# Kernel optimization log

Measured on AMD Instinct MI355X. Metric: run time of the kernel, lower is better.

The kernel has to match this reference:

```python
import jax, jax.numpy as jnp
import numpy as np


def setup_inputs() -> dict:
    key = jax.random.key(0)
    ks = jax.random.split(key, 5)
    B, C, H, W = 32, 32, 64, 64   # latent feature map (latent_space_channel_dim=32)
    D, K = 32, 512                # quant_dim, codebook_size
    return {
        "z": jax.random.normal(ks[0], (B, C, H, W), jnp.float32),
        "quant_w": jax.random.normal(ks[1], (D, C), jnp.float32) * 0.1,   # 1x1 conv kernel
        "quant_b": jnp.zeros((D,), jnp.float32),
        "codebook": jax.random.normal(ks[2], (K, D), jnp.float32),
        "post_quant_w": jax.random.normal(ks[3], (C, D), jnp.float32) * 0.1,
        "post_quant_b": jnp.zeros((C,), jnp.float32),
    }


def reference(z, quant_w, quant_b, codebook, post_quant_w, post_quant_b):
    B, C, H, W = z.shape
    D = quant_w.shape[0]
    # quant_conv: 1x1 conv == channel GEMM
    x = jnp.einsum('bchw,dc->bdhw', z, quant_w) + quant_b[None, :, None, None]
    # rearrange 'b c h w -> b c (h w)' then flatten tokens to [B*HW, D]
    xf = x.transpose(0, 2, 3, 1).reshape(-1, D)
    # squared euclidean distances to codebook (cdist**2), argmin, gather
    d2 = (jnp.sum(xf * xf, axis=-1, keepdims=True)
          - 2.0 * (xf @ codebook.T)
          + jnp.sum(codebook * codebook, axis=-1)[None, :])  # [B*HW, K]
    idx = jnp.argmin(d2, axis=-1)                              # [B*HW]
    q = codebook[idx]                                          # gather [B*HW, D]
    # commitment loss (encoder pull) + codebook loss (learnable codebook, no EMA)
    commit = jnp.mean((jax.lax.stop_gradient(q) - xf) ** 2)
    cb_loss = jnp.mean((q - jax.lax.stop_gradient(xf)) ** 2)
    loss = commit + cb_loss
    # straight-through estimator
    q_st = xf + jax.lax.stop_gradient(q - xf)
    qmap = q_st.reshape(B, H, W, D).transpose(0, 3, 1, 2)      # 'b c (h w) -> b c h w'
    # post_quant_conv: 1x1 conv back to latent channels
    out = jnp.einsum('bdhw,cd->bchw', qmap, post_quant_w) + post_quant_b[None, :, None, None]
    return out, idx.reshape(B, H * W), loss
```

## Files before the change

kernel.cpp:

```cpp
#include <hip/hip_runtime.h>

#define C_    32
#define D_    32
#define K_    512
#define HW_   4096
#define NTOK  131072
#define IDX_OFF   4194304
#define LOSS_OFF  4325376
#define TAU      2e-3f
#define CONS_EPS 1e-3f

#define WS_CBN   0
#define WS_CBH   4096
#define WS_CBL   36864
#define WS_XH    69632
#define WS_XL    8458240
#define WS_XFT   16846848
#define WS_IDXF  33624064
#define WS_BESTW 34148352
#define WS_NEEDED 34672640

typedef __attribute__((ext_vector_type(8))) __bf16 bf16x8;
typedef __attribute__((ext_vector_type(8))) short  short8;
typedef __attribute__((ext_vector_type(4))) float  f32x4;

__device__ inline unsigned short f2bf(float x) {
    unsigned u = __builtin_bit_cast(unsigned, x);
    return (unsigned short)((u + 0x7FFFu + ((u >> 16) & 1u)) >> 16);
}
__device__ inline float bf2f(unsigned short h) {
    unsigned u = ((unsigned)h) << 16; return __builtin_bit_cast(float, u);
}
__device__ inline bf16x8 ldfrag(const unsigned short* p) {
    return __builtin_bit_cast(bf16x8, *(const short8*)p);
}

__global__ __launch_bounds__(256)
void prep(const float* __restrict__ z,  const float* __restrict__ qw,
          const float* __restrict__ qb, const float* __restrict__ cb,
          float* __restrict__ cbn, unsigned short* __restrict__ cbh,
          unsigned short* __restrict__ cbl, unsigned short* __restrict__ xh,
          unsigned short* __restrict__ xl, float* __restrict__ xfT)
{
    const int tid = threadIdx.x;
    if (blockIdx.x == 0) {
        for (int k = tid; k < K_; k += 256) {
            const float* row = cb + k * D_;
            float s = 0.f; unsigned short hrow[32], lrow[32];
            #pragma unroll
            for (int d = 0; d < D_; ++d) {
                float v = row[d]; s = fmaf(v, v, s);
                unsigned short h = f2bf(v); hrow[d] = h; lrow[d] = f2bf(v - bf2f(h));
            }
            cbn[k] = s;
            #pragma unroll
            for (int j = 0; j < 4; ++j) {
                *(short8*)(cbh + k * 32 + 8 * j) = *(const short8*)(hrow + 8 * j);
                *(short8*)(cbl + k * 32 + 8 * j) = *(const short8*)(lrow + 8 * j);
            }
        }
    }
    const int token = blockIdx.x * 256 + tid;
    const int b = token >> 12, hw = token & (HW_ - 1);
    const float* zbase = z + (size_t)b * (C_ * HW_) + hw;
    float zv[C_];
    #pragma unroll
    for (int c = 0; c < C_; ++c) zv[c] = zbase[(size_t)c * HW_];
    unsigned short hrow[32], lrow[32];
    #pragma unroll
    for (int d = 0; d < D_; ++d) {
        float a = qb[d]; const float* qr = qw + d * C_;
        #pragma unroll
        for (int c = 0; c < C_; ++c) a = fmaf(zv[c], qr[c], a);
        xfT[(size_t)d * NTOK + token] = a;
        unsigned short h = f2bf(a); hrow[d] = h; lrow[d] = f2bf(a - bf2f(h));
    }
    #pragma unroll
    for (int j = 0; j < 4; ++j) {
        *(short8*)(xh + (size_t)token * 32 + 8 * j) = *(const short8*)(hrow + 8 * j);
        *(short8*)(xl + (size_t)token * 32 + 8 * j) = *(const short8*)(lrow + 8 * j);
    }
}

__global__ __launch_bounds__(256)
void scan_mfma(const unsigned short* __restrict__ xh, const unsigned short* __restrict__ xl,
               const unsigned short* __restrict__ cbh, const unsigned short* __restrict__ cbl,
               const float* __restrict__ cbn, unsigned* __restrict__ idxf,
               float* __restrict__ bestW)
{
    const int tid = threadIdx.x;
    const int wv = tid >> 6, l = tid & 63;
    const int tile = (blockIdx.x * 4 + wv) * 32;
    const int lr = l & 15, lg = l >> 4;

    const unsigned short* pa  = xh + (size_t)(tile + lr) * 32 + lg * 8;
    const unsigned short* pal = xl + (size_t)(tile + lr) * 32 + lg * 8;
    bf16x8 ah0 = ldfrag(pa),  ah1 = ldfrag(pa + 16 * 32);
    bf16x8 al0 = ldfrag(pal), al1 = ldfrag(pal + 16 * 32);

    float b1[8], b2[8]; int i1[8];
    #pragma unroll
    for (int s = 0; s < 8; ++s) { b1[s] = 3.4e38f; b2[s] = 3.4e38f; i1[s] = 0; }

    #pragma unroll 2
    for (int nt = 0; nt < 32; ++nt) {
        const size_t boff = (size_t)(nt * 16 + lr) * 32 + lg * 8;
        bf16x8 bh = ldfrag(cbh + boff);
        bf16x8 bl = ldfrag(cbl + boff);
        const float cn = cbn[nt * 16 + lr];
        f32x4 acc0 = {0.f, 0.f, 0.f, 0.f}, acc1 = {0.f, 0.f, 0.f, 0.f};
        acc0 = __builtin_amdgcn_mfma_f32_16x16x32_bf16(ah0, bh, acc0, 0, 0, 0);
        acc0 = __builtin_amdgcn_mfma_f32_16x16x32_bf16(ah0, bl, acc0, 0, 0, 0);
        acc0 = __builtin_amdgcn_mfma_f32_16x16x32_bf16(al0, bh, acc0, 0, 0, 0);
        acc1 = __builtin_amdgcn_mfma_f32_16x16x32_bf16(ah1, bh, acc1, 0, 0, 0);
        acc1 = __builtin_amdgcn_mfma_f32_16x16x32_bf16(ah1, bl, acc1, 0, 0, 0);
        acc1 = __builtin_amdgcn_mfma_f32_16x16x32_bf16(al1, bh, acc1, 0, 0, 0);
        const int n = nt * 16 + lr;
        #pragma unroll
        for (int r = 0; r < 4; ++r) {
            {
                const float d2 = fmaf(-2.f, acc0[r], cn);
                const bool lt1 = d2 < b1[r], lt2 = d2 < b2[r];
                b2[r] = lt1 ? b1[r] : (lt2 ? d2 : b2[r]);
                b1[r] = lt1 ? d2 : b1[r];
                i1[r] = lt1 ? n  : i1[r];
            }
            {
                const float d2 = fmaf(-2.f, acc1[r], cn);
                const bool lt1 = d2 < b1[4+r], lt2 = d2 < b2[4+r];
                b2[4+r] = lt1 ? b1[4+r] : (lt2 ? d2 : b2[4+r]);
                b1[4+r] = lt1 ? d2 : b1[4+r];
                i1[4+r] = lt1 ? n  : i1[4+r];
            }
        }
    }
    #pragma unroll
    for (int mk = 1; mk < 16; mk <<= 1) {
        #pragma unroll
        for (int s = 0; s < 8; ++s) {
            const float ob1 = __shfl_xor(b1[s], mk);
            const int   oi1 = __shfl_xor(i1[s], mk);
            const float ob2 = __shfl_xor(b2[s], mk);
            const bool take = (ob1 < b1[s]) || (ob1 == b1[s] && oi1 < i1[s]);
            const float loser = take ? b1[s] : ob1;
            b1[s] = take ? ob1 : b1[s];
            i1[s] = take ? oi1 : i1[s];
            b2[s] = fminf(fminf(b2[s], ob2), loser);
        }
    }
    #pragma unroll
    for (int s = 0; s < 8; ++s) {
        if (lr == s) {
            const int token = tile + (s >> 2) * 16 + lg * 4 + (s & 3);
            const bool fl = (b2[s] - b1[s]) < TAU;
            idxf[token]  = (unsigned)i1[s] | (fl ? 0x80000000u : 0u);
            bestW[token] = b1[s];
        }
    }
}

__global__ __launch_bounds__(256)
void combine(const float* __restrict__ cb, const float* __restrict__ pw,
             const float* __restrict__ pb, const float* __restrict__ cbn,
             const float* __restrict__ xfT, const unsigned* __restrict__ idxf,
             const float* __restrict__ bestW, float* __restrict__ out)
{
    __shared__ float lsum[4];
    const int tid = threadIdx.x;
    const int token = blockIdx.x * 256 + tid;
    const int b = token >> 12, hw = token & (HW_ - 1);
    const int lane = tid & 63;

    const unsigned pf = idxf[token];
    int idx = (int)(pf & 511u);
    int flag = (int)(pf >> 31);

    float xf[D_];
    #pragma unroll
    for (int d = 0; d < D_; ++d) xf[d] = xfT[(size_t)d * NTOK + token];

    {
        const float* row = cb + (size_t)idx * D_;
        float p0 = 0.f, p1 = 0.f, p2 = 0.f, p3 = 0.f;
        #pragma unroll
        for (int d = 0; d < D_; d += 4) {
            p0 = fmaf(xf[d],   row[d],   p0); p1 = fmaf(xf[d+1], row[d+1], p1);
            p2 = fmaf(xf[d+2], row[d+2], p2); p3 = fmaf(xf[d+3], row[d+3], p3);
        }
        const float dd = fmaf(-2.f, (p0 + p1) + (p2 + p3), cbn[idx]);
        flag |= (fabsf(dd - bestW[token]) > CONS_EPS) ? 1 : 0;
    }

    unsigned long long m = __ballot(flag != 0);
    while (m) {
        const int j = __ffsll(m) - 1; m &= m - 1;
        const int tokj = blockIdx.x * 256 + (tid & ~63) + j;
        float xfj[D_];
        #pragma unroll
        for (int d = 0; d < D_; ++d) xfj[d] = xfT[(size_t)d * NTOK + tokj];
        float bb = 3.4e38f; int bi = 0;
        #pragma unroll
        for (int p = 0; p < 8; ++p) {
            const int c = lane + 64 * p;
            const float* row = cb + (size_t)c * D_;
            float p0 = 0.f, p1 = 0.f, p2 = 0.f, p3 = 0.f;
            #pragma unroll
            for (int d = 0; d < D_; d += 4) {
                p0 = fmaf(xfj[d],   row[d],   p0); p1 = fmaf(xfj[d+1], row[d+1], p1);
                p2 = fmaf(xfj[d+2], row[d+2], p2); p3 = fmaf(xfj[d+3], row[d+3], p3);
            }
            const float dd = fmaf(-2.f, (p0 + p1) + (p2 + p3), cbn[c]);
            if (dd < bb) { bb = dd; bi = c; }
        }
        #pragma unroll
        for (int s = 1; s < 64; s <<= 1) {
            const float ob = __shfl_xor(bb, s); const int oi = __shfl_xor(bi, s);
            if (ob < bb || (ob == bb && oi < bi)) { bb = ob; bi = oi; }
        }
        if (lane == j) idx = bi;
    }

    out[IDX_OFF + token] = (float)idx;

    const float* qrow = cb + (size_t)idx * D_;
    float qv[D_], l = 0.f;
    #pragma unroll
    for (int d = 0; d < D_; ++d) { qv[d] = qrow[d]; const float df = qv[d] - xf[d]; l = fmaf(df, df, l); }

    float* obase = out + (size_t)b * (C_ * HW_) + hw;
    #pragma unroll
    for (int c = 0; c < C_; ++c) {
        float a = pb[c]; const float* pr = pw + c * D_;
        #pragma unroll
        for (int d = 0; d < D_; ++d) a = fmaf(qv[d], pr[d], a);
        obase[(size_t)c * HW_] = a;
    }

    #pragma unroll
    for (int off = 32; off; off >>= 1) l += __shfl_down(l, off);
    const int wid = tid >> 6;
    if (lane == 0) lsum[wid] = l;
    __syncthreads();
    if (tid == 0)
        atomicAdd(out + LOSS_OFF, ((lsum[0] + lsum[1]) + (lsum[2] + lsum[3])) * (2.0f / (float)(NTOK * D_)));
}

__global__ __launch_bounds__(256)
void vq_mono(const float* __restrict__ z,  const float* __restrict__ qw,
             const float* __restrict__ qb, const float* __restrict__ cb,
             const float* __restrict__ pw, const float* __restrict__ pb,
             float* __restrict__ out)
{
    __shared__ float cbn_s[K_];
    __shared__ float lsum[4];
    const int tid = threadIdx.x;
    for (int k = tid; k < K_; k += 256) {
        const float* row = cb + k * D_;
        float s = 0.f;
        #pragma unroll
        for (int d = 0; d < D_; ++d) s = fmaf(row[d], row[d], s);
        cbn_s[k] = s;
    }
    __syncthreads();
    const int token = blockIdx.x * 256 + tid;
    const int b = token >> 12, hw = token & (HW_ - 1);
    const float* zbase = z + (size_t)b * C_ * HW_ + hw;
    float zv[C_];
    #pragma unroll
    for (int c = 0; c < C_; ++c) zv[c] = zbase[(size_t)c * HW_];
    float xf[D_];
    #pragma unroll
    for (int d = 0; d < D_; ++d) {
        float a = qb[d];
        #pragma unroll
        for (int c = 0; c < C_; ++c) a = fmaf(zv[c], qw[d * C_ + c], a);
        xf[d] = a;
    }
    float best = 3.4e38f; int bi = 0;
    #pragma unroll 2
    for (int k = 0; k < K_; ++k) {
        const float* row = cb + k * D_;
        float p0 = 0.f, p1 = 0.f, p2 = 0.f, p3 = 0.f;
        #pragma unroll
        for (int d = 0; d < D_; d += 4) {
            p0 = fmaf(xf[d+0], row[d+0], p0); p1 = fmaf(xf[d+1], row[d+1], p1);
            p2 = fmaf(xf[d+2], row[d+2], p2); p3 = fmaf(xf[d+3], row[d+3], p3);
        }
        const float s = fmaf(-2.f, (p0+p1)+(p2+p3), cbn_s[k]);
        if (s < best) { best = s; bi = k; }
    }
    out[IDX_OFF + token] = (float)bi;
    const float* qrow = cb + (size_t)bi * D_;
    float qv[D_];
    #pragma unroll
    for (int d = 0; d < D_; ++d) qv[d] = qrow[d];
    float l = 0.f;
    #pragma unroll
    for (int d = 0; d < D_; ++d) { const float df = qv[d] - xf[d]; l = fmaf(df, df, l); }
    float* obase = out + (size_t)b * C_ * HW_ + hw;
    #pragma unroll
    for (int c = 0; c < C_; ++c) {
        float a = pb[c];
        #pragma unroll
        for (int d = 0; d < D_; ++d) a = fmaf(qv[d], pw[c * D_ + d], a);
        obase[(size_t)c * HW_] = a;
    }
    #pragma unroll
    for (int off = 32; off; off >>= 1) l += __shfl_down(l, off);
    const int wid = tid >> 6, lane = tid & 63;
    if (lane == 0) lsum[wid] = l;
    __syncthreads();
    if (tid == 0) {
        const float t = (lsum[0] + lsum[1]) + (lsum[2] + lsum[3]);
        atomicAdd(out + LOSS_OFF, t * (2.0f / (float)(NTOK * D_)));
    }
}

extern "C" void kernel_launch(void* const* d_in, const int* in_sizes, int n_in,
                              void* d_out, int out_size, void* d_ws, size_t ws_size,
                              hipStream_t stream) {
    (void)in_sizes; (void)n_in; (void)out_size;
    const float* z  = (const float*)d_in[0];
    const float* qw = (const float*)d_in[1];
    const float* qb = (const float*)d_in[2];
    const float* cb = (const float*)d_in[3];
    const float* pw = (const float*)d_in[4];
    const float* pb = (const float*)d_in[5];
    float* out = (float*)d_out;

    hipMemsetAsync((char*)d_out + (size_t)LOSS_OFF * sizeof(float), 0, sizeof(float), stream);

    if (ws_size < (size_t)WS_NEEDED) {
        vq_mono<<<NTOK / 256, 256, 0, stream>>>(z, qw, qb, cb, pw, pb, out);
        return;
    }
    char* ws = (char*)d_ws;
    float*          cbn  = (float*)(ws + WS_CBN);
    unsigned short* cbh  = (unsigned short*)(ws + WS_CBH);
    unsigned short* cbl  = (unsigned short*)(ws + WS_CBL);
    unsigned short* xh   = (unsigned short*)(ws + WS_XH);
    unsigned short* xl   = (unsigned short*)(ws + WS_XL);
    float*          xfT  = (float*)(ws + WS_XFT);
    unsigned*       idxf = (unsigned*)(ws + WS_IDXF);
    float*          bstW = (float*)(ws + WS_BESTW);

    prep<<<NTOK / 256, 256, 0, stream>>>(z, qw, qb, cb, cbn, cbh, cbl, xh, xl, xfT);
    scan_mfma<<<NTOK / 128, 256, 0, stream>>>(xh, xl, cbh, cbl, cbn, idxf, bstW);
    combine<<<NTOK / 256, 256, 0, stream>>>(cb, pw, pb, cbn, xfT, idxf, bstW, out);
}
```

Baseline: 95.15 us.

## Fuse quant conv, MFMA codebook scan and post-quant conv into one kernel

```diff
diff --git a/kernel.cpp b/kernel.cpp
--- a/kernel.cpp
+++ b/kernel.cpp
@@ -7,18 +7,12 @@
 #define NTOK  131072
 #define IDX_OFF   4194304
 #define LOSS_OFF  4325376
-#define TAU      2e-3f
-#define CONS_EPS 1e-3f
+#define TAU   2e-3f
 
 #define WS_CBN   0
 #define WS_CBH   4096
 #define WS_CBL   36864
-#define WS_XH    69632
-#define WS_XL    8458240
-#define WS_XFT   16846848
-#define WS_IDXF  33624064
-#define WS_BESTW 34148352
-#define WS_NEEDED 34672640
+#define WS_NEEDED 69632
 
 typedef __attribute__((ext_vector_type(8))) __bf16 bf16x8;
 typedef __attribute__((ext_vector_type(8))) short  short8;
@@ -31,72 +25,81 @@
 __device__ inline float bf2f(unsigned short h) {
     unsigned u = ((unsigned)h) << 16; return __builtin_bit_cast(float, u);
 }
-__device__ inline bf16x8 ldfrag(const unsigned short* p) {
-    return __builtin_bit_cast(bf16x8, *(const short8*)p);
-}
 
 __global__ __launch_bounds__(256)
-void prep(const float* __restrict__ z,  const float* __restrict__ qw,
-          const float* __restrict__ qb, const float* __restrict__ cb,
-          float* __restrict__ cbn, unsigned short* __restrict__ cbh,
-          unsigned short* __restrict__ cbl, unsigned short* __restrict__ xh,
-          unsigned short* __restrict__ xl, float* __restrict__ xfT)
+void prep_cb(const float* __restrict__ cb, float* __restrict__ cbn,
+             unsigned short* __restrict__ cbh, unsigned short* __restrict__ cbl)
 {
-    const int tid = threadIdx.x;
-    if (blockIdx.x == 0) {
-        for (int k = tid; k < K_; k += 256) {
-            const float* row = cb + k * D_;
-            float s = 0.f; unsigned short hrow[32], lrow[32];
-            #pragma unroll
-            for (int d = 0; d < D_; ++d) {
-                float v = row[d]; s = fmaf(v, v, s);
-                unsigned short h = f2bf(v); hrow[d] = h; lrow[d] = f2bf(v - bf2f(h));
-            }
-            cbn[k] = s;
-            #pragma unroll
-            for (int j = 0; j < 4; ++j) {
-                *(short8*)(cbh + k * 32 + 8 * j) = *(const short8*)(hrow + 8 * j);
-                *(short8*)(cbl + k * 32 + 8 * j) = *(const short8*)(lrow + 8 * j);
-            }
-        }
-    }
-    const int token = blockIdx.x * 256 + tid;
-    const int b = token >> 12, hw = token & (HW_ - 1);
-    const float* zbase = z + (size_t)b * (C_ * HW_) + hw;
-    float zv[C_];
-    #pragma unroll
-    for (int c = 0; c < C_; ++c) zv[c] = zbase[(size_t)c * HW_];
-    unsigned short hrow[32], lrow[32];
+    const int k = blockIdx.x * 256 + threadIdx.x;
+    const float* row = cb + k * D_;
+    float s = 0.f;
+    unsigned short h[32], lo[32];
     #pragma unroll
     for (int d = 0; d < D_; ++d) {
-        float a = qb[d]; const float* qr = qw + d * C_;
-        #pragma unroll
-        for (int c = 0; c < C_; ++c) a = fmaf(zv[c], qr[c], a);
-        xfT[(size_t)d * NTOK + token] = a;
-        unsigned short h = f2bf(a); hrow[d] = h; lrow[d] = f2bf(a - bf2f(h));
-    }
+        const float v = row[d]; s = fmaf(v, v, s);
+        const unsigned short hh = f2bf(v);
+        h[d] = hh; lo[d] = f2bf(v - bf2f(hh));
+    }
+    cbn[k] = s;
     #pragma unroll
     for (int j = 0; j < 4; ++j) {
-        *(short8*)(xh + (size_t)token * 32 + 8 * j) = *(const short8*)(hrow + 8 * j);
-        *(short8*)(xl + (size_t)token * 32 + 8 * j) = *(const short8*)(lrow + 8 * j);
+        *(short8*)(cbh + k * 32 + 8 * j) = *(const short8*)(h  + 8 * j);
+        *(short8*)(cbl + k * 32 + 8 * j) = *(const short8*)(lo + 8 * j);
     }
 }
 
 __global__ __launch_bounds__(256)
-void scan_mfma(const unsigned short* __restrict__ xh, const unsigned short* __restrict__ xl,
-               const unsigned short* __restrict__ cbh, const unsigned short* __restrict__ cbl,
-               const float* __restrict__ cbn, unsigned* __restrict__ idxf,
-               float* __restrict__ bestW)
+void vq_fused(const float* __restrict__ z,  const float* __restrict__ qw,
+              const float* __restrict__ qb, const float* __restrict__ cb,
+              const float* __restrict__ pw, const float* __restrict__ pb,
+              const unsigned short* __restrict__ cbh, const unsigned short* __restrict__ cbl,
+              const float* __restrict__ cbn, float* __restrict__ out)
 {
+    __shared__ float xsh[4][32][33];
+    __shared__ int   si[4][32];
+    __shared__ float lsum[4];
+
     const int tid = threadIdx.x;
     const int wv = tid >> 6, l = tid & 63;
-    const int tile = (blockIdx.x * 4 + wv) * 32;
+    const int tok = l & 31, half = l >> 5;
+    const int T0 = blockIdx.x * 128 + wv * 32;
+    const int b = T0 >> 12, hw0 = T0 & (HW_ - 1);
+
+    {
+        const float* zbase = z + (size_t)b * (C_ * HW_) + hw0 + tok;
+        float zv[C_];
+        #pragma unroll
+        for (int c = 0; c < C_; ++c) zv[c] = zbase[(size_t)c * HW_];
+        #pragma unroll
+        for (int i = 0; i < 16; ++i) {
+            const int d = half * 16 + i;
+            float a = qb[d];
+            const float4* qr = (const float4*)(qw + d * C_);
+            #pragma unroll
+            for (int c4 = 0; c4 < 8; ++c4) {
+                const float4 q4 = qr[c4];
+                a = fmaf(zv[4*c4+0], q4.x, a); a = fmaf(zv[4*c4+1], q4.y, a);
+                a = fmaf(zv[4*c4+2], q4.z, a); a = fmaf(zv[4*c4+3], q4.w, a);
+            }
+            xsh[wv][tok][d] = a;
+        }
+    }
+    __syncthreads();
+
     const int lr = l & 15, lg = l >> 4;
-
-    const unsigned short* pa  = xh + (size_t)(tile + lr) * 32 + lg * 8;
-    const unsigned short* pal = xl + (size_t)(tile + lr) * 32 + lg * 8;
-    bf16x8 ah0 = ldfrag(pa),  ah1 = ldfrag(pa + 16 * 32);
-    bf16x8 al0 = ldfrag(pal), al1 = ldfrag(pal + 16 * 32);
+    short8 sh0, sl0, sh1, sl1;
+    #pragma unroll
+    for (int j = 0; j < 8; ++j) {
+        const float v0 = xsh[wv][lr][lg * 8 + j];
+        const float v1 = xsh[wv][16 + lr][lg * 8 + j];
+        const unsigned short a0 = f2bf(v0), a1 = f2bf(v1);
+        sh0[j] = (short)a0; sl0[j] = (short)f2bf(v0 - bf2f(a0));
+        sh1[j] = (short)a1; sl1[j] = (short)f2bf(v1 - bf2f(a1));
+    }
+    const bf16x8 ah0 = __builtin_bit_cast(bf16x8, sh0);
+    const bf16x8 al0 = __builtin_bit_cast(bf16x8, sl0);
+    const bf16x8 ah1 = __builtin_bit_cast(bf16x8, sh1);
+    const bf16x8 al1 = __builtin_bit_cast(bf16x8, sl1);
 
     float b1[8], b2[8]; int i1[8];
     #pragma unroll
@@ -105,10 +108,10 @@
     #pragma unroll 2
     for (int nt = 0; nt < 32; ++nt) {
         const size_t boff = (size_t)(nt * 16 + lr) * 32 + lg * 8;
-        bf16x8 bh = ldfrag(cbh + boff);
-        bf16x8 bl = ldfrag(cbl + boff);
+        const bf16x8 bh = __builtin_bit_cast(bf16x8, *(const short8*)(cbh + boff));
+        const bf16x8 bl = __builtin_bit_cast(bf16x8, *(const short8*)(cbl + boff));
         const float cn = cbn[nt * 16 + lr];
-        f32x4 acc0 = {0.f, 0.f, 0.f, 0.f}, acc1 = {0.f, 0.f, 0.f, 0.f};
+        f32x4 acc0 = {0.f,0.f,0.f,0.f}, acc1 = {0.f,0.f,0.f,0.f};
         acc0 = __builtin_amdgcn_mfma_f32_16x16x32_bf16(ah0, bh, acc0, 0, 0, 0);
         acc0 = __builtin_amdgcn_mfma_f32_16x16x32_bf16(ah0, bl, acc0, 0, 0, 0);
         acc0 = __builtin_amdgcn_mfma_f32_16x16x32_bf16(al0, bh, acc0, 0, 0, 0);
@@ -151,95 +154,83 @@
     #pragma unroll
     for (int s = 0; s < 8; ++s) {
         if (lr == s) {
-            const int token = tile + (s >> 2) * 16 + lg * 4 + (s & 3);
-            const bool fl = (b2[s] - b1[s]) < TAU;
-            idxf[token]  = (unsigned)i1[s] | (fl ? 0x80000000u : 0u);
-            bestW[token] = b1[s];
-        }
-    }
-}
-
-__global__ __launch_bounds__(256)
-void combine(const float* __restrict__ cb, const float* __restrict__ pw,
-             const float* __restrict__ pb, const float* __restrict__ cbn,
-             const float* __restrict__ xfT, const unsigned* __restrict__ idxf,
-             const float* __restrict__ bestW, float* __restrict__ out)
-{
-    __shared__ float lsum[4];
-    const int tid = threadIdx.x;
-    const int token = blockIdx.x * 256 + tid;
-    const int b = token >> 12, hw = token & (HW_ - 1);
-    const int lane = tid & 63;
-
-    const unsigned pf = idxf[token];
-    int idx = (int)(pf & 511u);
-    int flag = (int)(pf >> 31);
-
-    float xf[D_];
-    #pragma unroll
-    for (int d = 0; d < D_; ++d) xf[d] = xfT[(size_t)d * NTOK + token];
+            const int tokW = (s >> 2) * 16 + lg * 4 + (s & 3);
+            si[wv][tokW] = i1[s] | (((b2[s] - b1[s]) < TAU) ? 512 : 0);
+        }
+    }
+    __syncthreads();
 
     {
-        const float* row = cb + (size_t)idx * D_;
-        float p0 = 0.f, p1 = 0.f, p2 = 0.f, p3 = 0.f;
-        #pragma unroll
-        for (int d = 0; d < D_; d += 4) {
-            p0 = fmaf(xf[d],   row[d],   p0); p1 = fmaf(xf[d+1], row[d+1], p1);
-            p2 = fmaf(xf[d+2], row[d+2], p2); p3 = fmaf(xf[d+3], row[d+3], p3);
-        }
-        const float dd = fmaf(-2.f, (p0 + p1) + (p2 + p3), cbn[idx]);
-        flag |= (fabsf(dd - bestW[token]) > CONS_EPS) ? 1 : 0;
-    }
-
-    unsigned long long m = __ballot(flag != 0);
-    while (m) {
-        const int j = __ffsll(m) - 1; m &= m - 1;
-        const int tokj = blockIdx.x * 256 + (tid & ~63) + j;
-        float xfj[D_];
-        #pragma unroll
-        for (int d = 0; d < D_; ++d) xfj[d] = xfT[(size_t)d * NTOK + tokj];
-        float bb = 3.4e38f; int bi = 0;
-        #pragma unroll
-        for (int p = 0; p < 8; ++p) {
-            const int c = lane + 64 * p;
-            const float* row = cb + (size_t)c * D_;
-            float p0 = 0.f, p1 = 0.f, p2 = 0.f, p3 = 0.f;
+        const int v = si[wv][tok];
+        unsigned long long m = __ballot(half == 0 && (v & 512));
+        while (m) {
+            const int j = __ffsll(m) - 1; m &= m - 1;
+            float xfj[D_];
             #pragma unroll
-            for (int d = 0; d < D_; d += 4) {
-                p0 = fmaf(xfj[d],   row[d],   p0); p1 = fmaf(xfj[d+1], row[d+1], p1);
-                p2 = fmaf(xfj[d+2], row[d+2], p2); p3 = fmaf(xfj[d+3], row[d+3], p3);
-            }
-            const float dd = fmaf(-2.f, (p0 + p1) + (p2 + p3), cbn[c]);
-            if (dd < bb) { bb = dd; bi = c; }
-        }
-        #pragma unroll
-        for (int s = 1; s < 64; s <<= 1) {
-            const float ob = __shfl_xor(bb, s); const int oi = __shfl_xor(bi, s);
-            if (ob < bb || (ob == bb && oi < bi)) { bb = ob; bi = oi; }
-        }
-        if (lane == j) idx = bi;
-    }
-
-    out[IDX_OFF + token] = (float)idx;
-
-    const float* qrow = cb + (size_t)idx * D_;
-    float qv[D_], l = 0.f;
-    #pragma unroll
-    for (int d = 0; d < D_; ++d) { qv[d] = qrow[d]; const float df = qv[d] - xf[d]; l = fmaf(df, df, l); }
-
-    float* obase = out + (size_t)b * (C_ * HW_) + hw;
-    #pragma unroll
-    for (int c = 0; c < C_; ++c) {
-        float a = pb[c]; const float* pr = pw + c * D_;
-        #pragma unroll
-        for (int d = 0; d < D_; ++d) a = fmaf(qv[d], pr[d], a);
+            for (int d = 0; d < D_; ++d) xfj[d] = xsh[wv][j][d];
+            float bb = 3.4e38f; int bi = 0;
+            #pragma unroll
+            for (int p = 0; p < 8; ++p) {
+                const int c = l + 64 * p;
+                const float* row = cb + (size_t)c * D_;
+                float p0 = 0.f, p1 = 0.f, p2 = 0.f, p3 = 0.f;
+                #pragma unroll
+                for (int d = 0; d < D_; d += 4) {
+                    p0 = fmaf(xfj[d],   row[d],   p0); p1 = fmaf(xfj[d+1], row[d+1], p1);
+                    p2 = fmaf(xfj[d+2], row[d+2], p2); p3 = fmaf(xfj[d+3], row[d+3], p3);
+                }
+                const float dd = fmaf(-2.f, (p0 + p1) + (p2 + p3), cbn[c]);
+                if (dd < bb) { bb = dd; bi = c; }
+            }
+            #pragma unroll
+            for (int s = 1; s < 64; s <<= 1) {
+                const float ob = __shfl_xor(bb, s); const int oi = __shfl_xor(bi, s);
+                if (ob < bb || (ob == bb && oi < bi)) { bb = ob; bi = oi; }
+            }
+            if (l == j) si[wv][j] = bi;
+        }
+    }
+    __syncthreads();
+    const int myidx = si[wv][tok] & 511;
+
+    float qv[D_];
+    {
+        const float4* qrow = (const float4*)(cb + (size_t)myidx * D_);
+        #pragma unroll
+        for (int d4 = 0; d4 < 8; ++d4) {
+            const float4 t = qrow[d4];
+            qv[4*d4+0] = t.x; qv[4*d4+1] = t.y; qv[4*d4+2] = t.z; qv[4*d4+3] = t.w;
+        }
+    }
+    float lacc = 0.f;
+    if (half == 0) {
+        #pragma unroll
+        for (int d = 0; d < D_; ++d) {
+            const float df = qv[d] - xsh[wv][tok][d];
+            lacc = fmaf(df, df, lacc);
+        }
+        out[IDX_OFF + T0 + tok] = (float)myidx;
+    }
+    lacc += __shfl_down(lacc, 16); lacc += __shfl_down(lacc, 8);
+    lacc += __shfl_down(lacc, 4);  lacc += __shfl_down(lacc, 2);
+    lacc += __shfl_down(lacc, 1);
+    if (l == 0) lsum[wv] = lacc;
+
+    float* obase = out + (size_t)b * (C_ * HW_) + hw0 + tok;
+    #pragma unroll
+    for (int i = 0; i < 16; ++i) {
+        const int c = half * 16 + i;
+        float a = pb[c];
+        const float4* pr = (const float4*)(pw + c * D_);
+        #pragma unroll
+        for (int d4 = 0; d4 < 8; ++d4) {
+            const float4 p4 = pr[d4];
+            a = fmaf(qv[4*d4+0], p4.x, a); a = fmaf(qv[4*d4+1], p4.y, a);
+            a = fmaf(qv[4*d4+2], p4.z, a); a = fmaf(qv[4*d4+3], p4.w, a);
+        }
         obase[(size_t)c * HW_] = a;
     }
 
-    #pragma unroll
-    for (int off = 32; off; off >>= 1) l += __shfl_down(l, off);
-    const int wid = tid >> 6;
-    if (lane == 0) lsum[wid] = l;
     __syncthreads();
     if (tid == 0)
         atomicAdd(out + LOSS_OFF, ((lsum[0] + lsum[1]) + (lsum[2] + lsum[3])) * (2.0f / (float)(NTOK * D_)));
@@ -335,16 +326,10 @@
         return;
     }
     char* ws = (char*)d_ws;
-    float*          cbn  = (float*)(ws + WS_CBN);
-    unsigned short* cbh  = (unsigned short*)(ws + WS_CBH);
-    unsigned short* cbl  = (unsigned short*)(ws + WS_CBL);
-    unsigned short* xh   = (unsigned short*)(ws + WS_XH);
-    unsigned short* xl   = (unsigned short*)(ws + WS_XL);
-    float*          xfT  = (float*)(ws + WS_XFT);
-    unsigned*       idxf = (unsigned*)(ws + WS_IDXF);
-    float*          bstW = (float*)(ws + WS_BESTW);
-
-    prep<<<NTOK / 256, 256, 0, stream>>>(z, qw, qb, cb, cbn, cbh, cbl, xh, xl, xfT);
-    scan_mfma<<<NTOK / 128, 256, 0, stream>>>(xh, xl, cbh, cbl, cbn, idxf, bstW);
-    combine<<<NTOK / 256, 256, 0, stream>>>(cb, pw, pb, cbn, xfT, idxf, bstW, out);
-}
+    float*          cbn = (float*)(ws + WS_CBN);
+    unsigned short* cbh = (unsigned short*)(ws + WS_CBH);
+    unsigned short* cbl = (unsigned short*)(ws + WS_CBL);
+
+    prep_cb<<<2, 256, 0, stream>>>(cb, cbn, cbh, cbl);
+    vq_fused<<<NTOK / 128, 256, 0, stream>>>(z, qw, qb, cb, pw, pb, cbh, cbl, cbn, out);
+}
```

Result: slower. 107.6 us (+13.0%).
